# Optimization experiments

Measured on AMD Instinct MI355X. Metric: run time of the kernel, lower is better.

Reference implementation:

```python
import jax, jax.numpy as jnp
import numpy as np

N, F_IN, F_OUT = 8192, 256, 128


def setup_inputs() -> dict:
    key = jax.random.key(0)
    k1, k2, k3, k4 = jax.random.split(key, 4)
    h = jax.random.normal(k1, (N, F_IN), dtype=jnp.float32)
    adj = jax.random.randint(k2, (N, N), 0, 2, dtype=jnp.int32)
    # xavier-uniform-like init scales
    w_lim = float(np.sqrt(6.0 / (F_IN + F_OUT)))
    a_lim = float(np.sqrt(6.0 / (2 * F_OUT + 1)))
    W = jax.random.uniform(k3, (F_IN, F_OUT), jnp.float32, -w_lim, w_lim)
    a = jax.random.uniform(k4, (2 * F_OUT, 1), jnp.float32, -a_lim, a_lim)
    return {"h": h, "adj": adj, "W": W, "a": a}


def reference(h, adj, W, a):
    # Wh: [N, F_OUT]
    Wh = h @ W
    # Fused form of the pairwise-concat score: e[i,j] = leakyrelu(Wh_i.a1 + Wh_j.a2)
    a1 = a[:F_OUT]   # [F_OUT, 1]
    a2 = a[F_OUT:]   # [F_OUT, 1]
    s1 = Wh @ a1     # [N, 1]
    s2 = Wh @ a2     # [N, 1]
    e = jax.nn.leaky_relu(s1 + s2.T, negative_slope=0.2)  # [N, N]
    e = jnp.where(adj > 0, e, jnp.float32(-9e15))
    attention = jax.nn.softmax(e, axis=1)
    return attention @ Wh  # [N, F_OUT]
```

## Files before the change

kernel.cpp:

```cpp
#include <hip/hip_runtime.h>

#define N_   8192
#define FIN  256
#define FOUT 128

typedef _Float16 f16x8 __attribute__((ext_vector_type(8)));
typedef _Float16 f16x4 __attribute__((ext_vector_type(4)));
typedef float    f32x4 __attribute__((ext_vector_type(4)));

#define LDS_BARRIER() asm volatile("s_waitcnt lgkmcnt(0)\n\ts_barrier" ::: "memory")

__global__ __launch_bounds__(256) void k_wh(
    const float* __restrict__ h, const float* __restrict__ W,
    const float* __restrict__ a, float* __restrict__ Wh,
    float* __restrict__ s1, float* __restrict__ s2)
{
    __shared__ float hrow[2][FIN];
    __shared__ float rbuf[2][2][2];
    const int t   = threadIdx.x;
    const int rh  = t >> 7;
    const int c   = t & 127;
    const int row = (blockIdx.x << 1) + rh;

    hrow[rh][c]       = h[(size_t)row * FIN + c];
    hrow[rh][c + 128] = h[(size_t)row * FIN + c + 128];
    __syncthreads();

    float acc = 0.f;
    #pragma unroll 8
    for (int k = 0; k < FIN; ++k)
        acc = fmaf(hrow[rh][k], W[k * FOUT + c], acc);

    Wh[(size_t)row * FOUT + c] = acc;

    float p1 = acc * a[c];
    float p2 = acc * a[FOUT + c];
    #pragma unroll
    for (int off = 32; off; off >>= 1) {
        p1 += __shfl_down(p1, off, 64);
        p2 += __shfl_down(p2, off, 64);
    }
    if ((t & 63) == 0) { rbuf[rh][c >> 6][0] = p1; rbuf[rh][c >> 6][1] = p2; }
    __syncthreads();
    if (c == 0) {
        const float k2 = 1.44269504088896f;
        s1[row] = (rbuf[rh][0][0] + rbuf[rh][1][0]) * k2;
        s2[row] = (rbuf[rh][0][1] + rbuf[rh][1][1]) * k2;
    }
}

__global__ __launch_bounds__(256) void k_tr(
    const float* __restrict__ Wh, _Float16* __restrict__ WhT)
{
    __shared__ float tile[64][129];
    const int t = threadIdx.x;
    const int rbase = blockIdx.x * 64;

    #pragma unroll
    for (int q = 0; q < 8; ++q) {
        int i4 = q * 256 + t;
        int r  = i4 >> 5;
        int c4 = (i4 & 31) * 4;
        *(float4*)&tile[r][c4] = *(const float4*)&Wh[(size_t)(rbase + r) * FOUT + c4];
    }
    __syncthreads();

    const int c = t >> 1, half = t & 1;
    _Float16 buf[32];
    #pragma unroll
    for (int r = 0; r < 32; ++r) buf[r] = (_Float16)tile[32 * half + r][c];
    #pragma unroll
    for (int q = 0; q < 4; ++q)
        *(f16x8*)&WhT[(size_t)c * N_ + rbase + 32 * half + 8 * q] = *(f16x8*)&buf[8 * q];
}

__global__ __launch_bounds__(512, 4) void k_attn(
    const int* __restrict__ adj, const _Float16* __restrict__ WhT,
    const float* __restrict__ s1g, const float* __restrict__ s2g,
    float* __restrict__ num_g, float* __restrict__ den_g)
{
    __shared__ _Float16 pA[2][32][136];
    __shared__ float s2s[2048];

    const int t  = threadIdx.x;
    const int w  = t >> 6;
    const int l  = t & 63;

    const int rb    = blockIdx.x & 255;
    const int sp    = blockIdx.x >> 8;
    const int rbase = rb * 32;
    const int jbase = sp * 2048;

    *(float4*)&s2s[t * 4] = *(const float4*)&s2g[jbase + t * 4];

    const int r  = t >> 4;
    const int j0 = (t & 15) << 3;
    const float s1r = s1g[rbase + r];
    const int* __restrict__ arow = adj + (size_t)(rbase + r) * N_ + jbase;

    const int ln15 = l & 15, lq = l >> 4;
    const _Float16* __restrict__ bptr =
        WhT + (size_t)(16 * w + ln15) * N_ + jbase + 8 * lq;

    f32x4 acc0 = {0.f, 0.f, 0.f, 0.f};
    f32x4 acc1 = {0.f, 0.f, 0.f, 0.f};
    float denp = 0.f;

    auto computeP = [&](const int4& aA, const int4& aB, int tile, int buf) {
        const float bias = -5.77078016f;
        const float* s2p = &s2s[tile * 128 + j0];
        float4 sA = *(const float4*)(s2p);
        float4 sB = *(const float4*)(s2p + 4);
        float m, e;
        f16x8 pv;
        m = s1r + sA.x; e = fmaxf(m, 0.2f * m); pv[0] = (_Float16)(aA.x ? __builtin_amdgcn_exp2f(e + bias) : 0.f);
        m = s1r + sA.y; e = fmaxf(m, 0.2f * m); pv[1] = (_Float16)(aA.y ? __builtin_amdgcn_exp2f(e + bias) : 0.f);
        m = s1r + sA.z; e = fmaxf(m, 0.2f * m); pv[2] = (_Float16)(aA.z ? __builtin_amdgcn_exp2f(e + bias) : 0.f);
        m = s1r + sA.w; e = fmaxf(m, 0.2f * m); pv[3] = (_Float16)(aA.w ? __builtin_amdgcn_exp2f(e + bias) : 0.f);
        m = s1r + sB.x; e = fmaxf(m, 0.2f * m); pv[4] = (_Float16)(aB.x ? __builtin_amdgcn_exp2f(e + bias) : 0.f);
        m = s1r + sB.y; e = fmaxf(m, 0.2f * m); pv[5] = (_Float16)(aB.y ? __builtin_amdgcn_exp2f(e + bias) : 0.f);
        m = s1r + sB.z; e = fmaxf(m, 0.2f * m); pv[6] = (_Float16)(aB.z ? __builtin_amdgcn_exp2f(e + bias) : 0.f);
        m = s1r + sB.w; e = fmaxf(m, 0.2f * m); pv[7] = (_Float16)(aB.w ? __builtin_amdgcn_exp2f(e + bias) : 0.f);
        denp += (float)pv[0] + (float)pv[1] + (float)pv[2] + (float)pv[3]
              + (float)pv[4] + (float)pv[5] + (float)pv[6] + (float)pv[7];
        *(f16x8*)&pA[buf][r][j0] = pv;
    };

    auto mmaTile = [&](int buf, int jb) {
        f16x8 b0 = *(const f16x8*)(bptr + jb);
        f16x8 b1 = *(const f16x8*)(bptr + jb + 32);
        f16x8 b2 = *(const f16x8*)(bptr + jb + 64);
        f16x8 b3 = *(const f16x8*)(bptr + jb + 96);
        const _Float16* a0p = &pA[buf][ln15][8 * lq];
        const _Float16* a1p = &pA[buf][16 + ln15][8 * lq];
        acc0 = __builtin_amdgcn_mfma_f32_16x16x32_f16(*(const f16x8*)(a0p),      b0, acc0, 0, 0, 0);
        acc1 = __builtin_amdgcn_mfma_f32_16x16x32_f16(*(const f16x8*)(a1p),      b0, acc1, 0, 0, 0);
        acc0 = __builtin_amdgcn_mfma_f32_16x16x32_f16(*(const f16x8*)(a0p + 32), b1, acc0, 0, 0, 0);
        acc1 = __builtin_amdgcn_mfma_f32_16x16x32_f16(*(const f16x8*)(a1p + 32), b1, acc1, 0, 0, 0);
        acc0 = __builtin_amdgcn_mfma_f32_16x16x32_f16(*(const f16x8*)(a0p + 64), b2, acc0, 0, 0, 0);
        acc1 = __builtin_amdgcn_mfma_f32_16x16x32_f16(*(const f16x8*)(a1p + 64), b2, acc1, 0, 0, 0);
        acc0 = __builtin_amdgcn_mfma_f32_16x16x32_f16(*(const f16x8*)(a0p + 96), b3, acc0, 0, 0, 0);
        acc1 = __builtin_amdgcn_mfma_f32_16x16x32_f16(*(const f16x8*)(a1p + 96), b3, acc1, 0, 0, 0);
    };

    int4 av0A = *(const int4*)(arow + j0);
    int4 av0B = *(const int4*)(arow + j0 + 4);
    int4 av1A = *(const int4*)(arow + 128 + j0);
    int4 av1B = *(const int4*)(arow + 128 + j0 + 4);

    LDS_BARRIER();
    computeP(av0A, av0B, 0, 0);
    LDS_BARRIER();

    for (int tt = 0; tt < 14; tt += 2) {
        {
            const int tn = tt + 2;
            av0A = *(const int4*)(arow + tn * 128 + j0);
            av0B = *(const int4*)(arow + tn * 128 + j0 + 4);
            mmaTile(0, tt * 128);
            computeP(av1A, av1B, tt + 1, 1);
            LDS_BARRIER();
        }
        {
            const int tn = tt + 3;
            av1A = *(const int4*)(arow + tn * 128 + j0);
            av1B = *(const int4*)(arow + tn * 128 + j0 + 4);
            mmaTile(1, (tt + 1) * 128);
            computeP(av0A, av0B, tt + 2, 0);
            LDS_BARRIER();
        }
    }
    mmaTile(0, 14 * 128);
    computeP(av1A, av1B, 15, 1);
    LDS_BARRIER();
    mmaTile(1, 15 * 128);

    denp += __shfl_xor(denp, 1, 64);
    denp += __shfl_xor(denp, 2, 64);
    denp += __shfl_xor(denp, 4, 64);
    denp += __shfl_xor(denp, 8, 64);
    if ((t & 15) == 0)
        den_g[(size_t)sp * N_ + rbase + r] = denp;

    const int colg = 16 * w + ln15;
    const int rq   = lq * 4;
    #pragma unroll
    for (int q = 0; q < 4; ++q) {
        num_g[((size_t)sp * N_ + rbase + rq + q)      * FOUT + colg] = acc0[q];
        num_g[((size_t)sp * N_ + rbase + 16 + rq + q) * FOUT + colg] = acc1[q];
    }
}

__global__ __launch_bounds__(256) void k_norm(
    const float* __restrict__ num_g, const float* __restrict__ den_g,
    float* __restrict__ out)
{
    const int idx4 = blockIdx.x * 256 + threadIdx.x;
    const int i  = idx4 >> 5;
    const int c4 = (idx4 & 31) * 4;

    float4 s = {0.f, 0.f, 0.f, 0.f};
    float  d = 0.f;
    #pragma unroll
    for (int sp = 0; sp < 4; ++sp) {
        float4 v = *(const float4*)(num_g + ((size_t)sp * N_ + i) * FOUT + c4);
        s.x += v.x; s.y += v.y; s.z += v.z; s.w += v.w;
        d += den_g[(size_t)sp * N_ + i];
    }
    const float inv = 1.f / d;
    float4 o = {s.x * inv, s.y * inv, s.z * inv, s.w * inv};
    *(float4*)&out[(size_t)i * FOUT + c4] = o;
}

extern "C" void kernel_launch(void* const* d_in, const int* in_sizes, int n_in,
                              void* d_out, int out_size, void* d_ws, size_t ws_size,
                              hipStream_t stream) {
    const float* h   = (const float*)d_in[0];
    const int*   adj = (const int*)d_in[1];
    const float* W   = (const float*)d_in[2];
    const float* a   = (const float*)d_in[3];
    float* out = (float*)d_out;

    char* ws = (char*)d_ws;
    float*    Wh  = (float*)ws;
    _Float16* WhT = (_Float16*)(ws + (4u << 20));
    float*    s1  = (float*)(ws + (6u << 20));
    float*    s2  = (float*)(ws + (6u << 20) + 32768);
    float*    num = (float*)(ws + (7u << 20));
    float*    den = (float*)(ws + (23u << 20));

    k_wh  <<<N_ / 2, 256, 0, stream>>>(h, W, a, Wh, s1, s2);
    k_tr  <<<N_ / 64, 256, 0, stream>>>(Wh, WhT);
    k_attn<<<1024, 512, 0, stream>>>(adj, WhT, s1, s2, num, den);
    k_norm<<<1024, 256, 0, stream>>>(num, den, out);
}
```

Before: 131.9 us.

## Pack adjacency into a bitmask before the attention kernel

Adds a pre-pass kernel that compresses the int32 adjacency matrix into one bit per entry using wave shuffles. The attention kernel then reads a 32-bit mask word per tile instead of two int4 loads per thread. Adjacency still has to be read in full once by the pack kernel. The gain relies on separating the bandwidth-heavy streaming from the compute-heavy attention loop, at the cost of an extra launch and mask traffic.

```diff
diff --git a/kernel.cpp b/kernel.cpp
--- a/kernel.cpp
+++ b/kernel.cpp
@@ -3,12 +3,34 @@
 #define N_   8192
 #define FIN  256
 #define FOUT 128
+#define NW   (N_ / 32)
 
 typedef _Float16 f16x8 __attribute__((ext_vector_type(8)));
-typedef _Float16 f16x4 __attribute__((ext_vector_type(4)));
 typedef float    f32x4 __attribute__((ext_vector_type(4)));
+typedef unsigned int uint;
 
 #define LDS_BARRIER() asm volatile("s_waitcnt lgkmcnt(0)\n\ts_barrier" ::: "memory")
+
+__global__ __launch_bounds__(256) void k_pack(
+    const int* __restrict__ adj, uint* __restrict__ bm)
+{
+    const int wid = (blockIdx.x * 256 + threadIdx.x) >> 6;
+    const int l   = threadIdx.x & 63;
+    const int4* __restrict__ arow = (const int4*)(adj + (size_t)wid * N_);
+    uint* __restrict__ brow = bm + (size_t)wid * NW;
+
+    #pragma unroll 2
+    for (int jb = 0; jb < 32; ++jb) {
+        int4 av = arow[jb * 64 + l];
+        uint nib = (uint)(av.x != 0) | ((uint)(av.y != 0) << 1)
+                 | ((uint)(av.z != 0) << 2) | ((uint)(av.w != 0) << 3);
+        uint v = nib | (__shfl_xor(nib, 1, 64) << 4);
+        v = v | (__shfl_xor(v, 2, 64) << 8);
+        v = v | (__shfl_xor(v, 4, 64) << 16);
+        if ((l & 7) == 0)
+            brow[jb * 8 + (l >> 3)] = v;
+    }
+}
 
 __global__ __launch_bounds__(256) void k_wh(
     const float* __restrict__ h, const float* __restrict__ W,
@@ -75,7 +97,7 @@
 }
 
 __global__ __launch_bounds__(512, 4) void k_attn(
-    const int* __restrict__ adj, const _Float16* __restrict__ WhT,
+    const uint* __restrict__ bm, const _Float16* __restrict__ WhT,
     const float* __restrict__ s1g, const float* __restrict__ s2g,
     float* __restrict__ num_g, float* __restrict__ den_g)
 {
@@ -94,9 +116,12 @@
     *(float4*)&s2s[t * 4] = *(const float4*)&s2g[jbase + t * 4];
 
     const int r  = t >> 4;
-    const int j0 = (t & 15) << 3;
+    const int g  = t & 15;
+    const int j0 = g << 3;
+    const int shift = (g & 3) * 8;
     const float s1r = s1g[rbase + r];
-    const int* __restrict__ arow = adj + (size_t)(rbase + r) * N_ + jbase;
+    const uint* __restrict__ brow =
+        bm + (size_t)(rbase + r) * NW + sp * 64 + (g >> 2);
 
     const int ln15 = l & 15, lq = l >> 4;
     const _Float16* __restrict__ bptr =
@@ -106,21 +131,22 @@
     f32x4 acc1 = {0.f, 0.f, 0.f, 0.f};
     float denp = 0.f;
 
-    auto computeP = [&](const int4& aA, const int4& aB, int tile, int buf) {
+    auto computeP = [&](uint mv, int tile, int buf) {
         const float bias = -5.77078016f;
+        const uint byte = mv >> shift;
         const float* s2p = &s2s[tile * 128 + j0];
         float4 sA = *(const float4*)(s2p);
         float4 sB = *(const float4*)(s2p + 4);
         float m, e;
         f16x8 pv;
-        m = s1r + sA.x; e = fmaxf(m, 0.2f * m); pv[0] = (_Float16)(aA.x ? __builtin_amdgcn_exp2f(e + bias) : 0.f);
-        m = s1r + sA.y; e = fmaxf(m, 0.2f * m); pv[1] = (_Float16)(aA.y ? __builtin_amdgcn_exp2f(e + bias) : 0.f);
-        m = s1r + sA.z; e = fmaxf(m, 0.2f * m); pv[2] = (_Float16)(aA.z ? __builtin_amdgcn_exp2f(e + bias) : 0.f);
-        m = s1r + sA.w; e = fmaxf(m, 0.2f * m); pv[3] = (_Float16)(aA.w ? __builtin_amdgcn_exp2f(e + bias) : 0.f);
-        m = s1r + sB.x; e = fmaxf(m, 0.2f * m); pv[4] = (_Float16)(aB.x ? __builtin_amdgcn_exp2f(e + bias) : 0.f);
-        m = s1r + sB.y; e = fmaxf(m, 0.2f * m); pv[5] = (_Float16)(aB.y ? __builtin_amdgcn_exp2f(e + bias) : 0.f);
-        m = s1r + sB.z; e = fmaxf(m, 0.2f * m); pv[6] = (_Float16)(aB.z ? __builtin_amdgcn_exp2f(e + bias) : 0.f);
-        m = s1r + sB.w; e = fmaxf(m, 0.2f * m); pv[7] = (_Float16)(aB.w ? __builtin_amdgcn_exp2f(e + bias) : 0.f);
+        m = s1r + sA.x; e = fmaxf(m, 0.2f * m); pv[0] = (_Float16)((byte & 1u)   ? __builtin_amdgcn_exp2f(e + bias) : 0.f);
+        m = s1r + sA.y; e = fmaxf(m, 0.2f * m); pv[1] = (_Float16)((byte & 2u)   ? __builtin_amdgcn_exp2f(e + bias) : 0.f);
+        m = s1r + sA.z; e = fmaxf(m, 0.2f * m); pv[2] = (_Float16)((byte & 4u)   ? __builtin_amdgcn_exp2f(e + bias) : 0.f);
+        m = s1r + sA.w; e = fmaxf(m, 0.2f * m); pv[3] = (_Float16)((byte & 8u)   ? __builtin_amdgcn_exp2f(e + bias) : 0.f);
+        m = s1r + sB.x; e = fmaxf(m, 0.2f * m); pv[4] = (_Float16)((byte & 16u)  ? __builtin_amdgcn_exp2f(e + bias) : 0.f);
+        m = s1r + sB.y; e = fmaxf(m, 0.2f * m); pv[5] = (_Float16)((byte & 32u)  ? __builtin_amdgcn_exp2f(e + bias) : 0.f);
+        m = s1r + sB.z; e = fmaxf(m, 0.2f * m); pv[6] = (_Float16)((byte & 64u)  ? __builtin_amdgcn_exp2f(e + bias) : 0.f);
+        m = s1r + sB.w; e = fmaxf(m, 0.2f * m); pv[7] = (_Float16)((byte & 128u) ? __builtin_amdgcn_exp2f(e + bias) : 0.f);
         denp += (float)pv[0] + (float)pv[1] + (float)pv[2] + (float)pv[3]
               + (float)pv[4] + (float)pv[5] + (float)pv[6] + (float)pv[7];
         *(f16x8*)&pA[buf][r][j0] = pv;
@@ -143,35 +169,29 @@
         acc1 = __builtin_amdgcn_mfma_f32_16x16x32_f16(*(const f16x8*)(a1p + 96), b3, acc1, 0, 0, 0);
     };
 
-    int4 av0A = *(const int4*)(arow + j0);
-    int4 av0B = *(const int4*)(arow + j0 + 4);
-    int4 av1A = *(const int4*)(arow + 128 + j0);
-    int4 av1B = *(const int4*)(arow + 128 + j0 + 4);
+    uint mv0 = brow[0];
+    uint mv1 = brow[4];
 
     LDS_BARRIER();
-    computeP(av0A, av0B, 0, 0);
+    computeP(mv0, 0, 0);
     LDS_BARRIER();
 
     for (int tt = 0; tt < 14; tt += 2) {
         {
-            const int tn = tt + 2;
-            av0A = *(const int4*)(arow + tn * 128 + j0);
-            av0B = *(const int4*)(arow + tn * 128 + j0 + 4);
+            mv0 = brow[(tt + 2) * 4];
             mmaTile(0, tt * 128);
-            computeP(av1A, av1B, tt + 1, 1);
+            computeP(mv1, tt + 1, 1);
             LDS_BARRIER();
         }
         {
-            const int tn = tt + 3;
-            av1A = *(const int4*)(arow + tn * 128 + j0);
-            av1B = *(const int4*)(arow + tn * 128 + j0 + 4);
+            mv1 = brow[(tt + 3) * 4];
             mmaTile(1, (tt + 1) * 128);
-            computeP(av0A, av0B, tt + 2, 0);
+            computeP(mv0, tt + 2, 0);
             LDS_BARRIER();
         }
     }
     mmaTile(0, 14 * 128);
-    computeP(av1A, av1B, 15, 1);
+    computeP(mv1, 15, 1);
     LDS_BARRIER();
     mmaTile(1, 15 * 128);
 
@@ -228,9 +248,11 @@
     float*    s2  = (float*)(ws + (6u << 20) + 32768);
     float*    num = (float*)(ws + (7u << 20));
     float*    den = (float*)(ws + (23u << 20));
-
+    uint*     bmk = (uint*)(ws + (24u << 20));
+
+    k_pack<<<2048,   256, 0, stream>>>(adj, bmk);
     k_wh  <<<N_ / 2, 256, 0, stream>>>(h, W, a, Wh, s1, s2);
     k_tr  <<<N_ / 64, 256, 0, stream>>>(Wh, WhT);
-    k_attn<<<1024, 512, 0, stream>>>(adj, WhT, s1, s2, num, den);
-    k_norm<<<1024, 256, 0, stream>>>(num, den, out);
-}
+    k_attn<<<1024,  512, 0, stream>>>(bmk, WhT, s1, s2, num, den);
+    k_norm<<<1024,  256, 0, stream>>>(num, den, out);
+}
```

Result: slower. 162.7 us (+23.3%).
